# Kernel tuning notes

Hardware: AMD Instinct MI355X
Metric: run time of the kernel (lower is better)

## Reference

```python
import jax, jax.numpy as jnp
import numpy as np

B, S, E = 4, 2048, 2048
H = 16
DH = 2048 // H  # head dim = 128


def setup_inputs() -> dict:
    key = jax.random.key(0)
    k0, k1, k2, k3 = jax.random.split(key, 4)
    scale = 1.0 / np.sqrt(E)
    embedded = jax.random.normal(k0, (B, S, E), dtype=jnp.float32)
    # stacked per-head projection weights, bias-free Linear: y = x @ W^T -> store as [H, E, DH]
    Wq = jax.random.normal(k1, (H, E, DH), dtype=jnp.float32) * scale
    Wk = jax.random.normal(k2, (H, E, DH), dtype=jnp.float32) * scale
    Wv = jax.random.normal(k3, (H, E, DH), dtype=jnp.float32) * scale
    return {"embedded": embedded, "Wq": Wq, "Wk": Wk, "Wv": Wv}


def reference(embedded, Wq, Wk, Wv):
    # batched over heads instead of the original python loop (same math)
    q = jnp.einsum("bse,hed->bhsd", embedded, Wq)
    k = jnp.einsum("bse,hed->bhsd", embedded, Wk)
    v = jnp.einsum("bse,hed->bhsd", embedded, Wv)
    scores = jnp.einsum("bhsd,bhtd->bhst", q, k) / jnp.sqrt(jnp.float32(DH))
    causal = jnp.tril(jnp.ones((S, S), dtype=bool))  # [S, S]
    scores = jnp.where(causal, scores, -jnp.inf)
    probs = jax.nn.softmax(scores, axis=-1)
    out = jnp.einsum("bhst,bhtd->bhsd", probs, v)
    cated = out.transpose(0, 2, 1, 3).reshape(B, S, H * DH)  # concat heads on dim=2
    return jnp.round(cated, 4)
```

## Files before the change

kernel.cpp:

```cpp
#include <hip/hip_runtime.h>

typedef float   f32x4 __attribute__((ext_vector_type(4)));
typedef _Float16 half8 __attribute__((ext_vector_type(8)));
typedef _Float16 half4 __attribute__((ext_vector_type(4)));

#define B_  4
#define S_  2048
#define E_  2048
#define H_  16
#define DH_ 128

__device__ __forceinline__ void gld16(const void* g, void* l) {
  __builtin_amdgcn_global_load_lds((const void __attribute__((address_space(1)))*)g,
                                   (void __attribute__((address_space(3)))*)l, 16, 0, 0);
}

__global__ __launch_bounds__(256) void k_prep(const float* __restrict__ X, _Float16* __restrict__ Xh,
    const float* __restrict__ Wq, const float* __restrict__ Wk, const float* __restrict__ Wv,
    _Float16* __restrict__ Wqt, _Float16* __restrict__ Wkt, _Float16* __restrict__ Wvt) {
  const int bid = blockIdx.x;
  const int tid = threadIdx.x;
  if (bid < 8192) {
    size_t i = ((size_t)bid * 256 + tid) * 8;
    float4 a = *(const float4*)(X + i);
    float4 b = *(const float4*)(X + i + 4);
    half8 h;
    h[0]=(_Float16)a.x; h[1]=(_Float16)a.y; h[2]=(_Float16)a.z; h[3]=(_Float16)a.w;
    h[4]=(_Float16)b.x; h[5]=(_Float16)b.y; h[6]=(_Float16)b.z; h[7]=(_Float16)b.w;
    *(half8*)(Xh + i) = h;
  } else {
    __shared__ float t[32][33];
    const int wi = bid - 8192;
    const int e0 = (wi & 63) * 32;
    const int d0 = ((wi >> 6) & 3) * 32;
    const int pz = wi >> 8;
    const int p = pz >> 4, h = pz & 15;
    const float* W  = (p==0) ? Wq  : (p==1) ? Wk  : Wv;
    _Float16*    Wt = (p==0) ? Wqt : (p==1) ? Wkt : Wvt;
    const int tx = tid & 31, ty = tid >> 5;
    for (int i=0;i<4;i++)
      t[ty+8*i][tx] = W[((size_t)h*E_ + (e0+ty+8*i))*DH_ + d0+tx];
    __syncthreads();
    for (int i=0;i<4;i++)
      Wt[((size_t)h*DH_ + (d0+ty+8*i))*E_ + e0+tx] = (_Float16)t[tx][ty+8*i];
  }
}

#define NT 64

__global__ __launch_bounds__(512, 2) void k_gemm(const _Float16* __restrict__ X,
    const _Float16* __restrict__ Wq, const _Float16* __restrict__ Wk, const _Float16* __restrict__ Wv,
    _Float16* __restrict__ Qo, _Float16* __restrict__ Ko, _Float16* __restrict__ Vt)
{
  __shared__ __align__(16) _Float16 pool[32768];

  const int z = blockIdx.z;
  const _Float16* Wp = (z==0) ? Wq : (z==1) ? Wk : Wv;

  const int fi  = blockIdx.x + (blockIdx.y << 5);
  const int xcd = fi & 7, kk_ = fi >> 3;
  const int lbx = ((xcd >> 1) << 3) | (kk_ & 7);
  const int lby = ((xcd & 1) << 2) | (kk_ >> 3);
  const int m0 = lbx << 8, n0 = lby << 8;

  const int tid = threadIdx.x;
  const int wid = tid >> 6, lane = tid & 63, quad = lane >> 4, lcol = lane & 15;
  const int wm = wid >> 2, wn = wid & 3;

  const int r8_  = tid >> 3;
  const int s_   = (tid & 7) ^ (r8_ & 7);
  const int srow = 2*r8_ + (s_ >> 2);
  const int soff = srow * E_ + (s_ & 3) * 8;
  const int sldsb = wid * 1024;

  const _Float16* Ag = X  + (size_t)m0 * E_;
  const _Float16* Bg = Wp + (size_t)n0 * E_;

  auto stA = [&](int mh, int tt, int buf){
    gld16(Ag + (size_t)mh*(128*E_) + tt*32 + soff,
          (char*)pool + buf*32768 + mh*8192 + sldsb);
  };
  auto stB = [&](int nh, int tt, int buf){
    gld16(Bg + (size_t)nh*(128*E_) + tt*32 + soff,
          (char*)pool + buf*32768 + (2+nh)*8192 + sldsb);
  };

  half8 fa0[4], fa1[4], fb0[2], fb1[2];
  f32x4 acc[2][2][4][2] = {};

  const int lrow = lcol >> 1;
  const int pos  = (quad + ((lcol & 1) << 2)) ^ (lrow & 7);

  auto rdA = [&](half8* d, int mh, int buf){
    const _Float16* base = pool + buf*16384 + mh*4096;
    #pragma unroll
    for (int mi=0; mi<4; mi++)
      d[mi] = *(const half8*)(base + (wm*32 + mi*8 + lrow)*64 + pos*8);
  };
  auto rdB = [&](half8* d, int nh, int buf){
    const _Float16* base = pool + buf*16384 + (2+nh)*4096;
    #pragma unroll
    for (int ni=0; ni<2; ni++)
      d[ni] = *(const half8*)(base + (wn*16 + ni*8 + lrow)*64 + pos*8);
  };
  auto mm = [&](f32x4 (&ac)[4][2], const half8* av, const half8* bv){
    #pragma unroll
    for (int mi=0; mi<4; mi++)
      #pragma unroll
      for (int ni=0; ni<2; ni++)
        ac[mi][ni] = __builtin_amdgcn_mfma_f32_16x16x32_f16(av[mi], bv[ni], ac[mi][ni], 0, 0, 0);
  };

#define WOPEN() do{ __builtin_amdgcn_s_barrier(); \
    asm volatile("s_waitcnt lgkmcnt(0)" ::: "memory"); \
    __builtin_amdgcn_sched_barrier(0); }while(0)
#define SB() __builtin_amdgcn_sched_barrier(0)
#define PRIO1() __builtin_amdgcn_s_setprio(1)
#define PRIO0() __builtin_amdgcn_s_setprio(0)

#define TILE_EVEN(T, G1, G2, VM) do{ \
     \
    WOPEN(); rdB(fb1, 1, 0); SB(); \
    PRIO1(); mm(acc[0][0], fa0, fb0); PRIO0(); \
    if (G1) stB(0, (T)+1, 1); \
     \
    WOPEN(); rdA(fa1, 1, 0); SB(); \
    PRIO1(); mm(acc[0][1], fa0, fb1); PRIO0(); \
    if (G2) stA(0, (T)+2, 0); \
     \
    WOPEN(); \
    PRIO1(); mm(acc[1][1], fa1, fb1); PRIO0(); \
    if (G2) stB(1, (T)+2, 0); \
     \
    if (VM == 2)      { asm volatile("s_waitcnt vmcnt(2)" ::: "memory"); } \
    else if (VM == 0) { asm volatile("s_waitcnt vmcnt(0)" ::: "memory"); } \
    WOPEN(); \
    if (G1) { rdA(fa0, 0, 1); rdB(fb1, 1, 1); } SB(); \
    PRIO1(); mm(acc[1][0], fa1, fb0); PRIO0(); \
    if (G2) stA(1, (T)+2, 0); \
  }while(0)

#define TILE_ODD(T, G1, G2, VM) do{ \
     \
    WOPEN(); rdB(fb0, 0, 1); SB(); \
    PRIO1(); mm(acc[0][1], fa0, fb1); PRIO0(); \
    if (G1) stB(0, (T)+1, 0); \
     \
    WOPEN(); rdA(fa1, 1, 1); SB(); \
    PRIO1(); mm(acc[0][0], fa0, fb0); PRIO0(); \
    if (G2) stA(0, (T)+2, 1); \
     \
    WOPEN(); \
    PRIO1(); mm(acc[1][0], fa1, fb0); PRIO0(); \
    if (G2) stB(1, (T)+2, 1); \
     \
    if (VM == 2)      { asm volatile("s_waitcnt vmcnt(2)" ::: "memory"); } \
    else if (VM == 0) { asm volatile("s_waitcnt vmcnt(0)" ::: "memory"); } \
    WOPEN(); \
    if (G1) { rdA(fa0, 0, 0); rdB(fb0, 0, 0); } SB(); \
    PRIO1(); mm(acc[1][1], fa1, fb1); PRIO0(); \
    if (G2) stA(1, (T)+2, 1); \
  }while(0)

  stA(0,0,0); stB(0,0,0); stA(1,0,0); stB(1,0,0);
  stA(0,1,1); stB(1,1,1);
  asm volatile("s_waitcnt vmcnt(2)" ::: "memory");
  stA(1,1,1);
  __builtin_amdgcn_s_barrier();
  rdA(fa0, 0, 0); rdB(fb0, 0, 0);

  for (int t = 0; t < NT-4; t += 2){
    TILE_EVEN(t,   1, 1, 2);
    TILE_ODD (t+1, 1, 1, 2);
  }
  TILE_EVEN(NT-4, 1, 1, 2);
  TILE_ODD (NT-3, 1, 1, 2);
  TILE_EVEN(NT-2, 1, 0, 0);
  TILE_ODD (NT-1, 0, 0, -1);

#undef TILE_EVEN
#undef TILE_ODD
#undef WOPEN
#undef SB
#undef PRIO1
#undef PRIO0

  const int bb = m0 >> 11;
  const int s0 = m0 & 2047;
  const int h0 = n0 >> 7;
  if (z < 2){
    _Float16* O = z ? Ko : Qo;
    #pragma unroll
    for (int mh=0; mh<2; mh++)
      #pragma unroll
      for (int nh=0; nh<2; nh++)
        #pragma unroll
        for (int mi=0; mi<4; mi++)
          #pragma unroll
          for (int ni=0; ni<2; ni++){
            const int srw = s0 + mh*128 + wm*64 + mi*16 + quad*4;
            const int d = wn*32 + ni*16 + lcol;
            _Float16* p = O + (((size_t)bb*H_ + (h0+nh))*S_ + srw)*DH_ + d;
            const f32x4 v = acc[mh][nh][mi][ni];
            p[0]=(_Float16)v[0]; p[DH_]=(_Float16)v[1]; p[2*DH_]=(_Float16)v[2]; p[3*DH_]=(_Float16)v[3];
          }
  } else {
    #pragma unroll
    for (int mh=0; mh<2; mh++)
      #pragma unroll
      for (int nh=0; nh<2; nh++)
        #pragma unroll
        for (int mi=0; mi<4; mi++)
          #pragma unroll
          for (int ni=0; ni<2; ni++){
            const int scol = s0 + mh*128 + wm*64 + mi*16 + quad*4;
            const int d = wn*32 + ni*16 + lcol;
            const f32x4 u = acc[mh][nh][mi][ni];
            half4 v;
            v[0]=(_Float16)u[0]; v[1]=(_Float16)u[1]; v[2]=(_Float16)u[2]; v[3]=(_Float16)u[3];
            *(half4*)(Vt + (((size_t)bb*H_ + (h0+nh))*DH_ + d)*S_ + scol) = v;
          }
  }
}

__global__ __launch_bounds__(512, 2) void k_attn(const _Float16* __restrict__ Q,
    const _Float16* __restrict__ K, const _Float16* __restrict__ Vt, float* __restrict__ out)
{
  __shared__ __align__(16) _Float16 Ks[2][8192], Vs[2][8192];

  const int b = blockIdx.z, h = blockIdx.y;
  const int qsel = (b < 2) ? (7 - (int)blockIdx.x) : (int)blockIdx.x;
  const int q0 = qsel * 256;
  const int tid = threadIdx.x, wid = tid >> 6, lane = tid & 63, quad = lane >> 4, lcol = lane & 15;
  const size_t bh = (size_t)b*H_ + h;
  const _Float16* Qg = Q  + (bh*S_ + q0)*DH_;
  const _Float16* Kg = K  + bh*S_*DH_;
  const _Float16* Vg = Vt + bh*DH_*S_;

  int krow[2], kcg[2], vdr[2], vcg[2];
  for (int r=0;r<2;r++){
    int chunk = wid*128 + r*64 + lane;
    krow[r] = chunk >> 4;
    kcg[r]  = (chunk & 15) ^ (krow[r] & 15);
    vdr[r]  = chunk >> 3;
    vcg[r]  = (chunk & 7) ^ (vdr[r] & 7);
  }

  half8 qf[2][4];
  for (int g=0; g<2; g++)
    for (int kk=0; kk<4; kk++)
      qf[g][kk] = *(const half8*)(Qg + (size_t)(wid*32 + g*16 + lcol)*DH_ + kk*32 + quad*8);

  for (int r=0;r<2;r++){
    gld16(Kg + (size_t)krow[r]*DH_ + kcg[r]*8, (char*)Ks[0] + wid*2048 + r*1024 + lane*16);
    gld16(Vg + (size_t)vdr[r]*S_ + 0 + vcg[r]*8, (char*)Vs[0] + wid*2048 + r*1024 + lane*16);
  }

  f32x4 oaccT[2][8] = {};
  f32x4 lacc[2] = {};
  const half4 ones = {(_Float16)1.f,(_Float16)1.f,(_Float16)1.f,(_Float16)1.f};
  const float c1 = 0.12751879526654326f;
  const float c2 = -11.541560327111707f;
  const int rbase = q0 + wid*32;
  const int nt = (q0 >> 6) + 4;

  for (int t = 0; t < nt; t++) {
    const int buf = t & 1;
    const _Float16* ksb = Ks[buf];
    const _Float16* vsb = Vs[buf];
    const int j0 = t << 6;
    const bool live0 = (j0 <= rbase + 15);
    const bool live1 = (j0 <= rbase + 31);
    __syncthreads();

    f32x4 sa[2][4] = {};
    if (live0){
      __builtin_amdgcn_s_setprio(1);
      for (int kk=0; kk<4; kk++){
        int cl = (kk*4 + quad) ^ lcol;
        for (int jb=0; jb<4; jb++){
          half8 kf = *(const half8*)(ksb + (size_t)(jb*16 + lcol)*DH_ + cl*8);
          sa[0][jb] = __builtin_amdgcn_mfma_f32_16x16x32_f16(kf, qf[0][kk], sa[0][jb], 0, 0, 0);
          sa[1][jb] = __builtin_amdgcn_mfma_f32_16x16x32_f16(kf, qf[1][kk], sa[1][jb], 0, 0, 0);
        }
      }
      __builtin_amdgcn_s_setprio(0);
    } else if (live1){
      __builtin_amdgcn_s_setprio(1);
      for (int kk=0; kk<4; kk++){
        int cl = (kk*4 + quad) ^ lcol;
        for (int jb=0; jb<4; jb++){
          half8 kf = *(const half8*)(ksb + (size_t)(jb*16 + lcol)*DH_ + cl*8);
          sa[1][jb] = __builtin_amdgcn_mfma_f32_16x16x32_f16(kf, qf[1][kk], sa[1][jb], 0, 0, 0);
        }
      }
      __builtin_amdgcn_s_setprio(0);
    }

    if (t+1 < nt){
      const int j1 = (t+1) << 6;
      for (int r=0;r<2;r++){
        gld16(Kg + (size_t)(j1+krow[r])*DH_ + kcg[r]*8, (char*)Ks[buf^1] + wid*2048 + r*1024 + lane*16);
        gld16(Vg + (size_t)vdr[r]*S_ + j1 + vcg[r]*8,   (char*)Vs[buf^1] + wid*2048 + r*1024 + lane*16);
      }
    }

    if (live1){
      half4 pb[2][4];
      auto sm = [&](f32x4 (&s4)[4], half4 (&p4)[4], int rb){
        if (j0 + 63 > rb){
          for (int jb=0; jb<4; jb++)
            for (int rg=0; rg<4; rg++){
              int j = jb*16 + quad*4 + rg;
              float p = (j0 + j > rb + lcol) ? 0.f
                      : __builtin_amdgcn_exp2f(fmaf(s4[jb][rg], c1, c2));
              p4[jb][rg] = (_Float16)p;
            }
        } else {
          for (int jb=0; jb<4; jb++)
            for (int rg=0; rg<4; rg++)
              p4[jb][rg] = (_Float16)__builtin_amdgcn_exp2f(fmaf(s4[jb][rg], c1, c2));
        }
      };

      if (live0){
        sm(sa[0], pb[0], rbase);
        sm(sa[1], pb[1], rbase + 16);
        __builtin_amdgcn_s_setprio(1);
        for (int jb=0; jb<4; jb++){
          lacc[0] = __builtin_amdgcn_mfma_f32_16x16x16f16(ones, pb[0][jb], lacc[0], 0, 0, 0);
          lacc[1] = __builtin_amdgcn_mfma_f32_16x16x16f16(ones, pb[1][jb], lacc[1], 0, 0, 0);
        }
        for (int dblk=0; dblk<8; dblk++){
          const _Float16* vrow = vsb + (size_t)(dblk*16 + lcol)*64;
          for (int jb=0; jb<4; jb++){
            int cl = (2*jb + (quad>>1)) ^ (lcol & 7);
            half4 va = *(const half4*)(vrow + cl*8 + (quad&1)*4);
            oaccT[0][dblk] = __builtin_amdgcn_mfma_f32_16x16x16f16(va, pb[0][jb], oaccT[0][dblk], 0, 0, 0);
            oaccT[1][dblk] = __builtin_amdgcn_mfma_f32_16x16x16f16(va, pb[1][jb], oaccT[1][dblk], 0, 0, 0);
          }
        }
        __builtin_amdgcn_s_setprio(0);
      } else {
        sm(sa[1], pb[1], rbase + 16);
        __builtin_amdgcn_s_setprio(1);
        for (int jb=0; jb<4; jb++)
          lacc[1] = __builtin_amdgcn_mfma_f32_16x16x16f16(ones, pb[1][jb], lacc[1], 0, 0, 0);
        for (int dblk=0; dblk<8; dblk++){
          const _Float16* vrow = vsb + (size_t)(dblk*16 + lcol)*64;
          for (int jb=0; jb<4; jb++){
            int cl = (2*jb + (quad>>1)) ^ (lcol & 7);
            half4 va = *(const half4*)(vrow + cl*8 + (quad&1)*4);
            oaccT[1][dblk] = __builtin_amdgcn_mfma_f32_16x16x16f16(va, pb[1][jb], oaccT[1][dblk], 0, 0, 0);
          }
        }
        __builtin_amdgcn_s_setprio(0);
      }
    }
  }

  for (int g=0; g<2; g++){
    const float rinv = 1.f / lacc[g][0];
    const int s = q0 + wid*32 + g*16 + lcol;
    float* op = out + ((size_t)b*S_ + s)*(H_*DH_) + h*DH_ + quad*4;
    for (int dblk=0; dblk<8; dblk++){
      float4 v;
      v.x = oaccT[g][dblk][0]*rinv; v.y = oaccT[g][dblk][1]*rinv;
      v.z = oaccT[g][dblk][2]*rinv; v.w = oaccT[g][dblk][3]*rinv;
      *(float4*)(op + dblk*16) = v;
    }
  }
}

extern "C" void kernel_launch(void* const* d_in, const int* in_sizes, int n_in,
                              void* d_out, int out_size, void* d_ws, size_t ws_size,
                              hipStream_t stream) {
  const float* X  = (const float*)d_in[0];
  const float* Wq = (const float*)d_in[1];
  const float* Wk = (const float*)d_in[2];
  const float* Wv = (const float*)d_in[3];
  float* out = (float*)d_out;

  _Float16* Xh  = (_Float16*)d_ws;
  _Float16* Wqt = Xh  + (size_t)B_*S_*E_;
  _Float16* Wkt = Wqt + (size_t)H_*E_*DH_;
  _Float16* Wvt = Wkt + (size_t)H_*E_*DH_;
  _Float16* Qh  = Wvt + (size_t)H_*E_*DH_;
  _Float16* Kh  = Qh  + (size_t)B_*H_*S_*DH_;
  _Float16* Vth = Kh  + (size_t)B_*H_*S_*DH_;

  k_prep<<<8192 + 12288, 256, 0, stream>>>(X, Xh, Wq, Wk, Wv, Wqt, Wkt, Wvt);
  k_gemm<<<dim3(32, 8, 3), 512, 0, stream>>>(Xh, Wqt, Wkt, Wvt, Qh, Kh, Vth);
  k_attn<<<dim3(S_/256, H_, B_), 512, 0, stream>>>(Qh, Kh, Vth, out);
}
```

Before: 440.6 us.

## Shrink attention query tile to 128 rows and remap blocks by XCD

The attention kernel now gives each wave 16 query rows instead of 32, so a block covers 128 queries and the grid doubles to 1024 one-dimensional blocks. Block indices are remapped so that each XCD handles contiguous (batch, head) pairs, which should improve L2 reuse of K/V. Launch bounds rise to 4 blocks per CU to raise occupancy. The cost is that each K/V tile loaded into LDS is reused by half as many query rows, so more global/LDS traffic per FLOP, and the old per-batch reversal for causal load balancing is dropped.

```diff
diff --git a/kernel.cpp b/kernel.cpp
--- a/kernel.cpp
+++ b/kernel.cpp
@@ -223,19 +223,21 @@
   }
 }
 
-__global__ __launch_bounds__(512, 2) void k_attn(const _Float16* __restrict__ Q,
+__global__ __launch_bounds__(512, 4) void k_attn(const _Float16* __restrict__ Q,
     const _Float16* __restrict__ K, const _Float16* __restrict__ Vt, float* __restrict__ out)
 {
   __shared__ __align__(16) _Float16 Ks[2][8192], Vs[2][8192];
 
-  const int b = blockIdx.z, h = blockIdx.y;
-  const int qsel = (b < 2) ? (7 - (int)blockIdx.x) : (int)blockIdx.x;
-  const int q0 = qsel * 256;
+  const int f = blockIdx.x;
+  const int xcd = f & 7, sblk = f >> 3;
+  const int bh = xcd * 8 + (sblk >> 4);
+  const int b = bh >> 4, h = bh & 15;
+  const int q0 = (sblk & 15) * 128;
   const int tid = threadIdx.x, wid = tid >> 6, lane = tid & 63, quad = lane >> 4, lcol = lane & 15;
-  const size_t bh = (size_t)b*H_ + h;
-  const _Float16* Qg = Q  + (bh*S_ + q0)*DH_;
-  const _Float16* Kg = K  + bh*S_*DH_;
-  const _Float16* Vg = Vt + bh*DH_*S_;
+  const size_t bhs = (size_t)b*H_ + h;
+  const _Float16* Qg = Q  + (bhs*S_ + q0)*DH_;
+  const _Float16* Kg = K  + bhs*S_*DH_;
+  const _Float16* Vg = Vt + bhs*DH_*S_;
 
   int krow[2], kcg[2], vdr[2], vcg[2];
   for (int r=0;r<2;r++){
@@ -246,52 +248,39 @@
     vcg[r]  = (chunk & 7) ^ (vdr[r] & 7);
   }
 
-  half8 qf[2][4];
-  for (int g=0; g<2; g++)
-    for (int kk=0; kk<4; kk++)
-      qf[g][kk] = *(const half8*)(Qg + (size_t)(wid*32 + g*16 + lcol)*DH_ + kk*32 + quad*8);
+  half8 qf[4];
+  for (int kk=0; kk<4; kk++)
+    qf[kk] = *(const half8*)(Qg + (size_t)(wid*16 + lcol)*DH_ + kk*32 + quad*8);
 
   for (int r=0;r<2;r++){
     gld16(Kg + (size_t)krow[r]*DH_ + kcg[r]*8, (char*)Ks[0] + wid*2048 + r*1024 + lane*16);
     gld16(Vg + (size_t)vdr[r]*S_ + 0 + vcg[r]*8, (char*)Vs[0] + wid*2048 + r*1024 + lane*16);
   }
 
-  f32x4 oaccT[2][8] = {};
-  f32x4 lacc[2] = {};
+  f32x4 oaccT[8] = {};
+  f32x4 lacc = {};
   const half4 ones = {(_Float16)1.f,(_Float16)1.f,(_Float16)1.f,(_Float16)1.f};
   const float c1 = 0.12751879526654326f;
   const float c2 = -11.541560327111707f;
-  const int rbase = q0 + wid*32;
-  const int nt = (q0 >> 6) + 4;
+  const int rbase = q0 + wid*16;
+  const int nt = (q0 >> 6) + 2;
 
   for (int t = 0; t < nt; t++) {
     const int buf = t & 1;
     const _Float16* ksb = Ks[buf];
     const _Float16* vsb = Vs[buf];
     const int j0 = t << 6;
-    const bool live0 = (j0 <= rbase + 15);
-    const bool live1 = (j0 <= rbase + 31);
+    const bool live = (j0 <= rbase + 15);
     __syncthreads();
 
-    f32x4 sa[2][4] = {};
-    if (live0){
+    f32x4 sa[4] = {};
+    if (live){
       __builtin_amdgcn_s_setprio(1);
       for (int kk=0; kk<4; kk++){
         int cl = (kk*4 + quad) ^ lcol;
         for (int jb=0; jb<4; jb++){
           half8 kf = *(const half8*)(ksb + (size_t)(jb*16 + lcol)*DH_ + cl*8);
-          sa[0][jb] = __builtin_amdgcn_mfma_f32_16x16x32_f16(kf, qf[0][kk], sa[0][jb], 0, 0, 0);
-          sa[1][jb] = __builtin_amdgcn_mfma_f32_16x16x32_f16(kf, qf[1][kk], sa[1][jb], 0, 0, 0);
-        }
-      }
-      __builtin_amdgcn_s_setprio(0);
-    } else if (live1){
-      __builtin_amdgcn_s_setprio(1);
-      for (int kk=0; kk<4; kk++){
-        int cl = (kk*4 + quad) ^ lcol;
-        for (int jb=0; jb<4; jb++){
-          half8 kf = *(const half8*)(ksb + (size_t)(jb*16 + lcol)*DH_ + cl*8);
-          sa[1][jb] = __builtin_amdgcn_mfma_f32_16x16x32_f16(kf, qf[1][kk], sa[1][jb], 0, 0, 0);
+          sa[jb] = __builtin_amdgcn_mfma_f32_16x16x32_f16(kf, qf[kk], sa[jb], 0, 0, 0);
         }
       }
       __builtin_amdgcn_s_setprio(0);
@@ -305,70 +294,46 @@
       }
     }
 
-    if (live1){
-      half4 pb[2][4];
-      auto sm = [&](f32x4 (&s4)[4], half4 (&p4)[4], int rb){
-        if (j0 + 63 > rb){
-          for (int jb=0; jb<4; jb++)
-            for (int rg=0; rg<4; rg++){
-              int j = jb*16 + quad*4 + rg;
-              float p = (j0 + j > rb + lcol) ? 0.f
-                      : __builtin_amdgcn_exp2f(fmaf(s4[jb][rg], c1, c2));
-              p4[jb][rg] = (_Float16)p;
-            }
-        } else {
-          for (int jb=0; jb<4; jb++)
-            for (int rg=0; rg<4; rg++)
-              p4[jb][rg] = (_Float16)__builtin_amdgcn_exp2f(fmaf(s4[jb][rg], c1, c2));
+    if (live){
+      half4 pb[4];
+      if (j0 + 63 > rbase){
+        for (int jb=0; jb<4; jb++)
+          for (int rg=0; rg<4; rg++){
+            int j = jb*16 + quad*4 + rg;
+            float p = (j0 + j > rbase + lcol) ? 0.f
+                    : __builtin_amdgcn_exp2f(fmaf(sa[jb][rg], c1, c2));
+            pb[jb][rg] = (_Float16)p;
+          }
+      } else {
+        for (int jb=0; jb<4; jb++)
+          for (int rg=0; rg<4; rg++)
+            pb[jb][rg] = (_Float16)__builtin_amdgcn_exp2f(fmaf(sa[jb][rg], c1, c2));
+      }
+
+      __builtin_amdgcn_s_setprio(1);
+      for (int jb=0; jb<4; jb++)
+        lacc = __builtin_amdgcn_mfma_f32_16x16x16f16(ones, pb[jb], lacc, 0, 0, 0);
+
+      for (int dblk=0; dblk<8; dblk++){
+        const _Float16* vrow = vsb + (size_t)(dblk*16 + lcol)*64;
+        for (int jb=0; jb<4; jb++){
+          int cl = (2*jb + (quad>>1)) ^ (lcol & 7);
+          half4 va = *(const half4*)(vrow + cl*8 + (quad&1)*4);
+          oaccT[dblk] = __builtin_amdgcn_mfma_f32_16x16x16f16(va, pb[jb], oaccT[dblk], 0, 0, 0);
         }
-      };
-
-      if (live0){
-        sm(sa[0], pb[0], rbase);
-        sm(sa[1], pb[1], rbase + 16);
-        __builtin_amdgcn_s_setprio(1);
-        for (int jb=0; jb<4; jb++){
-          lacc[0] = __builtin_amdgcn_mfma_f32_16x16x16f16(ones, pb[0][jb], lacc[0], 0, 0, 0);
-          lacc[1] = __builtin_amdgcn_mfma_f32_16x16x16f16(ones, pb[1][jb], lacc[1], 0, 0, 0);
-        }
-        for (int dblk=0; dblk<8; dblk++){
-          const _Float16* vrow = vsb + (size_t)(dblk*16 + lcol)*64;
-          for (int jb=0; jb<4; jb++){
-            int cl = (2*jb + (quad>>1)) ^ (lcol & 7);
-            half4 va = *(const half4*)(vrow + cl*8 + (quad&1)*4);
-            oaccT[0][dblk] = __builtin_amdgcn_mfma_f32_16x16x16f16(va, pb[0][jb], oaccT[0][dblk], 0, 0, 0);
-            oaccT[1][dblk] = __builtin_amdgcn_mfma_f32_16x16x16f16(va, pb[1][jb], oaccT[1][dblk], 0, 0, 0);
-          }
-        }
-        __builtin_amdgcn_s_setprio(0);
-      } else {
-        sm(sa[1], pb[1], rbase + 16);
-        __builtin_amdgcn_s_setprio(1);
-        for (int jb=0; jb<4; jb++)
-          lacc[1] = __builtin_amdgcn_mfma_f32_16x16x16f16(ones, pb[1][jb], lacc[1], 0, 0, 0);
-        for (int dblk=0; dblk<8; dblk++){
-          const _Float16* vrow = vsb + (size_t)(dblk*16 + lcol)*64;
-          for (int jb=0; jb<4; jb++){
-            int cl = (2*jb + (quad>>1)) ^ (lcol & 7);
-            half4 va = *(const half4*)(vrow + cl*8 + (quad&1)*4);
-            oaccT[1][dblk] = __builtin_amdgcn_mfma_f32_16x16x16f16(va, pb[1][jb], oaccT[1][dblk], 0, 0, 0);
-          }
-        }
-        __builtin_amdgcn_s_setprio(0);
       }
+      __builtin_amdgcn_s_setprio(0);
     }
   }
 
-  for (int g=0; g<2; g++){
-    const float rinv = 1.f / lacc[g][0];
-    const int s = q0 + wid*32 + g*16 + lcol;
-    float* op = out + ((size_t)b*S_ + s)*(H_*DH_) + h*DH_ + quad*4;
-    for (int dblk=0; dblk<8; dblk++){
-      float4 v;
-      v.x = oaccT[g][dblk][0]*rinv; v.y = oaccT[g][dblk][1]*rinv;
-      v.z = oaccT[g][dblk][2]*rinv; v.w = oaccT[g][dblk][3]*rinv;
-      *(float4*)(op + dblk*16) = v;
-    }
+  const float rinv = 1.f / lacc[0];
+  const int srow = q0 + wid*16 + lcol;
+  float* op = out + ((size_t)b*S_ + srow)*(H_*DH_) + h*DH_ + quad*4;
+  for (int dblk=0; dblk<8; dblk++){
+    float4 v;
+    v.x = oaccT[dblk][0]*rinv; v.y = oaccT[dblk][1]*rinv;
+    v.z = oaccT[dblk][2]*rinv; v.w = oaccT[dblk][3]*rinv;
+    *(float4*)(op + dblk*16) = v;
   }
 }
 
@@ -391,5 +356,5 @@
 
   k_prep<<<8192 + 12288, 256, 0, stream>>>(X, Xh, Wq, Wk, Wv, Wqt, Wkt, Wvt);
   k_gemm<<<dim3(32, 8, 3), 512, 0, stream>>>(Xh, Wqt, Wkt, Wvt, Qh, Kh, Vth);
-  k_attn<<<dim3(S_/256, H_, B_), 512, 0, stream>>>(Qh, Kh, Vth, out);
-}
+  k_attn<<<1024, 512, 0, stream>>>(Qh, Kh, Vth, out);
+}
```

Measured after the change: 477.4 us. +8.3%, slower.
